# Performance work log

Measured on AMD Instinct MI355X. Metric: run time of the kernel, lower is better.

## Reference

```python
import jax, jax.numpy as jnp
import numpy as np

E, K, N, T = 8, 2048, 1024, 4096


def setup_inputs() -> dict:
    key = jax.random.key(0)
    kx, kw = jax.random.split(key)
    x = jax.random.normal(kx, (T, K), dtype=jnp.float32)
    weight = jax.random.normal(kw, (E, N, K), dtype=jnp.float32)
    # cumulative group end offsets per expert; equal split, offs[-1] == T
    offs = (jnp.arange(1, E + 1) * (T // E)).astype(jnp.int32)
    return {"x": x, "weight": weight, "offs": offs}


def reference(x, weight, offs):
    # torch: wt = weight.transpose(-2, -1); y = torch._grouped_mm(x, wt, offs)
    # Grouped GEMM over contiguous ragged token groups: tokens in
    # [starts[e], offs[e]) are multiplied by expert e's weight.
    wt = jnp.swapaxes(weight, -2, -1)  # [E, K, N]
    starts = jnp.concatenate([jnp.zeros((1,), offs.dtype), offs[:-1]])  # [E]
    tok = jnp.arange(x.shape[0], dtype=offs.dtype)[:, None]  # [T, 1]
    y = jnp.zeros((x.shape[0], wt.shape[-1]), dtype=x.dtype)
    for e in range(wt.shape[0]):  # fixed small expert count
        mask = (tok >= starts[e]) & (tok < offs[e])  # [T, 1]
        y = y + jnp.where(mask, x, jnp.zeros((), x.dtype)) @ wt[e]
    return y
```

## Files before the change

kernel.cpp:

```cpp
#include <hip/hip_runtime.h>
#include <hip/hip_bf16.h>

typedef __attribute__((ext_vector_type(4))) float f32x4;
typedef __attribute__((ext_vector_type(4))) unsigned int u32x4;
typedef __attribute__((ext_vector_type(8))) __bf16 bf16x8;

namespace {
constexpr int T_ = 4096;
constexpr int K_ = 2048;
constexpr int N_ = 1024;
constexpr int E_ = 8;
constexpr int BM = 128, BN = 128, BK = 32;
constexpr int LSTR = BK + 8;
constexpr size_t PART_ELEMS = (size_t)T_ * N_;
}

__device__ __forceinline__ unsigned int pk2(float a, float b) {
    union { __hip_bfloat162 h; unsigned int u; } c;
    c.h = __float22bfloat162_rn(make_float2(a, b));
    return c.u;
}

__device__ __forceinline__ u32x4 cvt8(f32x4 a, f32x4 b) {
    u32x4 r;
    r.x = pk2(a.x, a.y);
    r.y = pk2(a.z, a.w);
    r.z = pk2(b.x, b.y);
    r.w = pk2(b.z, b.w);
    return r;
}

template <int KSPLIT, int ATOMIC>
__global__ __launch_bounds__(256, 3) void gg_bf16_kernel(
        const float* __restrict__ x, const float* __restrict__ w,
        const int* __restrict__ offs, float* __restrict__ out) {
    constexpr int KCH = K_ / KSPLIT;
    constexpr int NKS = KCH / BK;
    __shared__ __align__(16) unsigned short As[2][BM * LSTR];
    __shared__ __align__(16) unsigned short Bs[2][BN * LSTR];

    const int tid = threadIdx.x;
    const int lane = tid & 63;
    const int wid = tid >> 6;
    const int wr = wid >> 1, wc = wid & 1;

    const int b = blockIdx.x;
    const int xcd = b & 7;
    const int inner = b >> 3;
    const int ks = inner >> 5;
    const int rem = inner & 31;
    const int by = xcd * 4 + (rem >> 3);
    const int bx = rem & 7;
    const int brow = by * BM;
    const int bcol = bx * BN;
    const int k0 = ks * KCH;

    float* outp = ATOMIC ? out : (out + (size_t)ks * PART_ELEMS);

    const int srow = tid >> 2;
    const int scol = (tid & 3) * 8;
    const float* aB0 = x + (size_t)(brow + srow) * K_ + k0 + scol;
    const float* aB1 = aB0 + (size_t)64 * K_;
    const int ldsO0 = srow * LSTR + scol;
    const int ldsO1 = (srow + 64) * LSTR + scol;

    const int frow = lane & 15;
    const int fk = (lane >> 4) * 8;
    const int aF = (wr * 64 + frow) * LSTR + fk;
    const int bF = (wc * 64 + frow) * LSTR + fk;

#define LOADT(t)                                                      \
    do {                                                              \
        const float* _a0 = aB0 + (t) * BK;                            \
        const float* _a1 = aB1 + (t) * BK;                            \
        const float* _b0 = bB0 + (t) * BK;                            \
        const float* _b1 = bB1 + (t) * BK;                            \
        ra0 = *(const f32x4*)_a0; ra1 = *(const f32x4*)(_a0 + 4);     \
        ra2 = *(const f32x4*)_a1; ra3 = *(const f32x4*)(_a1 + 4);     \
        rb0 = *(const f32x4*)_b0; rb1 = *(const f32x4*)(_b0 + 4);     \
        rb2 = *(const f32x4*)_b1; rb3 = *(const f32x4*)(_b1 + 4);     \
    } while (0)

#define STORET(buf)                                                   \
    do {                                                              \
        *(u32x4*)&As[buf][ldsO0] = cvt8(ra0, ra1);                    \
        *(u32x4*)&As[buf][ldsO1] = cvt8(ra2, ra3);                    \
        *(u32x4*)&Bs[buf][ldsO0] = cvt8(rb0, rb1);                    \
        *(u32x4*)&Bs[buf][ldsO1] = cvt8(rb2, rb3);                    \
    } while (0)

    for (int e = 0; e < E_; ++e) {
        const int s = (e == 0) ? 0 : offs[e - 1];
        const int en = offs[e];
        if (en <= brow || s >= brow + BM) continue;

        const float* bB0 = w + ((size_t)e * N_ + bcol + srow) * K_ + k0 + scol;
        const float* bB1 = bB0 + (size_t)64 * K_;

        f32x4 ra0, ra1, ra2, ra3, rb0, rb1, rb2, rb3;
        LOADT(0);
        STORET(0);
        LOADT(1);
        __syncthreads();

        f32x4 acc[4][4];
#pragma unroll
        for (int m = 0; m < 4; ++m)
#pragma unroll
            for (int n = 0; n < 4; ++n)
                acc[m][n] = f32x4{0.0f, 0.0f, 0.0f, 0.0f};

        for (int t = 0; t < NKS; ++t) {
            const int cur = t & 1;
            if (t + 1 < NKS) STORET(cur ^ 1);
            if (t + 2 < NKS) LOADT(t + 2);
            bf16x8 af[4], bg[4];
#pragma unroll
            for (int m = 0; m < 4; ++m)
                af[m] = *(const bf16x8*)&As[cur][aF + m * 16 * LSTR];
#pragma unroll
            for (int n = 0; n < 4; ++n)
                bg[n] = *(const bf16x8*)&Bs[cur][bF + n * 16 * LSTR];
#pragma unroll
            for (int m = 0; m < 4; ++m)
#pragma unroll
                for (int n = 0; n < 4; ++n)
                    acc[m][n] = __builtin_amdgcn_mfma_f32_16x16x32_bf16(
                        af[m], bg[n], acc[m][n], 0, 0, 0);
            __syncthreads();
        }

        const int cb = bcol + wc * 64 + frow;
#pragma unroll
        for (int m = 0; m < 4; ++m) {
            const int r0 = brow + wr * 64 + m * 16 + (lane >> 4) * 4;
#pragma unroll
            for (int r = 0; r < 4; ++r) {
                const int row = r0 + r;
                if (row < s || row >= en) continue;
                float* yp = outp + (size_t)row * N_ + cb;
#pragma unroll
                for (int n = 0; n < 4; ++n) {
                    if (ATOMIC) atomicAdd(&yp[n * 16], acc[m][n][r]);
                    else        yp[n * 16] = acc[m][n][r];
                }
            }
        }
        __syncthreads();
    }
#undef LOADT
#undef STORET
}

template <int P>
__global__ __launch_bounds__(256) void gg_reduce_kernel(
        const float* __restrict__ part, float* __restrict__ y) {
    const size_t i = (size_t)blockIdx.x * blockDim.x + threadIdx.x;
    f32x4 acc = ((const f32x4*)part)[i];
#pragma unroll
    for (int p = 1; p < P; ++p)
        acc += ((const f32x4*)(part + (size_t)p * PART_ELEMS))[i];
    ((f32x4*)y)[i] = acc;
}

extern "C" void kernel_launch(void* const* d_in, const int* in_sizes, int n_in,
                              void* d_out, int out_size, void* d_ws, size_t ws_size,
                              hipStream_t stream) {
    const float* x = (const float*)d_in[0];
    const float* w = (const float*)d_in[1];
    const int* offs = (const int*)d_in[2];
    float* y = (float*)d_out;
    float* part = (float*)d_ws;
    const int rgrid = (int)(PART_ELEMS / 4 / 256);

    if (ws_size >= 4 * PART_ELEMS * sizeof(float)) {
        gg_bf16_kernel<4, 0><<<dim3(256 * 4), dim3(256), 0, stream>>>(x, w, offs, part);
        gg_reduce_kernel<4><<<dim3(rgrid), dim3(256), 0, stream>>>(part, y);
    } else if (ws_size >= 2 * PART_ELEMS * sizeof(float)) {
        gg_bf16_kernel<2, 0><<<dim3(256 * 2), dim3(256), 0, stream>>>(x, w, offs, part);
        gg_reduce_kernel<2><<<dim3(rgrid), dim3(256), 0, stream>>>(part, y);
    } else {
        hipMemsetAsync(d_out, 0, PART_ELEMS * sizeof(float), stream);
        gg_bf16_kernel<2, 1><<<dim3(256 * 2), dim3(256), 0, stream>>>(x, w, offs, y);
    }
}
```

Before: 55.07 us.

## Pre-convert inputs to bf16 and stage tiles via direct global-to-LDS loads

```diff
diff --git a/kernel.cpp b/kernel.cpp
--- a/kernel.cpp
+++ b/kernel.cpp
@@ -4,6 +4,7 @@
 typedef __attribute__((ext_vector_type(4))) float f32x4;
 typedef __attribute__((ext_vector_type(4))) unsigned int u32x4;
 typedef __attribute__((ext_vector_type(8))) __bf16 bf16x8;
+using u16 = unsigned short;
 
 namespace {
 constexpr int T_ = 4096;
@@ -13,6 +14,8 @@
 constexpr int BM = 128, BN = 128, BK = 32;
 constexpr int LSTR = BK + 8;
 constexpr size_t PART_ELEMS = (size_t)T_ * N_;
+constexpr size_t XB_ELEMS = (size_t)T_ * K_;
+constexpr size_t WB_ELEMS = (size_t)E_ * N_ * K_;
 }
 
 __device__ __forceinline__ unsigned int pk2(float a, float b) {
@@ -30,14 +33,130 @@
     return r;
 }
 
+__device__ __forceinline__ void gld16(const u16* g, u16* l) {
+    __builtin_amdgcn_global_load_lds(
+        (const __attribute__((address_space(1))) void*)g,
+        (__attribute__((address_space(3))) void*)l, 16, 0, 0);
+}
+
+__global__ __launch_bounds__(256) void cvt_bf16_kernel(
+        const float* __restrict__ in, unsigned int* __restrict__ out, int n8) {
+    const int stride = gridDim.x * blockDim.x;
+    for (int i = blockIdx.x * blockDim.x + threadIdx.x; i < n8; i += stride) {
+        const f32x4 a = ((const f32x4*)in)[2 * i];
+        const f32x4 b = ((const f32x4*)in)[2 * i + 1];
+        ((u32x4*)out)[i] = cvt8(a, b);
+    }
+}
+
+template <int KSPLIT>
+__global__ __launch_bounds__(256) void gg_lds_kernel(
+        const u16* __restrict__ xb, const u16* __restrict__ wb,
+        const int* __restrict__ offs, float* __restrict__ out) {
+    constexpr int KCH = K_ / KSPLIT;
+    constexpr int NKS = KCH / BK;
+    __shared__ __align__(16) u16 As[2][BM * BK];
+    __shared__ __align__(16) u16 Bs[2][BN * BK];
+
+    const int tid = threadIdx.x;
+    const int lane = tid & 63;
+    const int wid = tid >> 6;
+    const int wr = wid >> 1, wc = wid & 1;
+
+    const int b = blockIdx.x;
+    const int xcd = b & 7;
+    const int inner = b >> 3;
+    const int ks = inner >> 5;
+    const int rem = inner & 31;
+    const int by = xcd * 4 + (rem >> 3);
+    const int bx = rem & 7;
+    const int brow = by * BM;
+    const int bcol = bx * BN;
+    const int k0 = ks * KCH;
+
+    float* outp = out + (size_t)ks * PART_ELEMS;
+
+    const int grow = tid >> 2;
+    const int gcol = (tid & 3) * 8;
+    const u16* aS = xb + (size_t)(brow + grow) * K_ + k0 + gcol;
+
+    const int frow = lane & 15;
+    const int fk = (lane >> 4) * 8;
+    const int aF = (wr * 64 + frow) * BK + fk;
+    const int bF = (wc * 64 + frow) * BK + fk;
+
+#define STAGE(t, buf)                                                  \
+    do {                                                               \
+        const u16* _a = aS + (t) * BK;                                 \
+        const u16* _b = bS + (t) * BK;                                 \
+        gld16(_a,                   &As[buf][tid * 8]);                \
+        gld16(_a + (size_t)64 * K_, &As[buf][2048 + tid * 8]);         \
+        gld16(_b,                   &Bs[buf][tid * 8]);                \
+        gld16(_b + (size_t)64 * K_, &Bs[buf][2048 + tid * 8]);         \
+    } while (0)
+
+    for (int e = 0; e < E_; ++e) {
+        const int s = (e == 0) ? 0 : offs[e - 1];
+        const int en = offs[e];
+        if (en <= brow || s >= brow + BM) continue;
+
+        const u16* bS = wb + ((size_t)e * N_ + bcol + grow) * K_ + k0 + gcol;
+
+        STAGE(0, 0);
+        __syncthreads();
+
+        f32x4 acc[4][4];
+#pragma unroll
+        for (int m = 0; m < 4; ++m)
+#pragma unroll
+            for (int n = 0; n < 4; ++n)
+                acc[m][n] = f32x4{0.0f, 0.0f, 0.0f, 0.0f};
+
+        for (int t = 0; t < NKS; ++t) {
+            const int cur = t & 1;
+            if (t + 1 < NKS) STAGE(t + 1, cur ^ 1);
+            bf16x8 af[4], bg[4];
+#pragma unroll
+            for (int m = 0; m < 4; ++m)
+                af[m] = *(const bf16x8*)&As[cur][aF + m * 16 * BK];
+#pragma unroll
+            for (int n = 0; n < 4; ++n)
+                bg[n] = *(const bf16x8*)&Bs[cur][bF + n * 16 * BK];
+#pragma unroll
+            for (int m = 0; m < 4; ++m)
+#pragma unroll
+                for (int n = 0; n < 4; ++n)
+                    acc[m][n] = __builtin_amdgcn_mfma_f32_16x16x32_bf16(
+                        af[m], bg[n], acc[m][n], 0, 0, 0);
+            __syncthreads();
+        }
+
+        const int cb = bcol + wc * 64 + frow;
+#pragma unroll
+        for (int m = 0; m < 4; ++m) {
+            const int r0 = brow + wr * 64 + m * 16 + (lane >> 4) * 4;
+#pragma unroll
+            for (int r = 0; r < 4; ++r) {
+                const int row = r0 + r;
+                if (row < s || row >= en) continue;
+                float* yp = outp + (size_t)row * N_ + cb;
+#pragma unroll
+                for (int n = 0; n < 4; ++n) yp[n * 16] = acc[m][n][r];
+            }
+        }
+        __syncthreads();
+    }
+#undef STAGE
+}
+
 template <int KSPLIT, int ATOMIC>
 __global__ __launch_bounds__(256, 3) void gg_bf16_kernel(
         const float* __restrict__ x, const float* __restrict__ w,
         const int* __restrict__ offs, float* __restrict__ out) {
     constexpr int KCH = K_ / KSPLIT;
     constexpr int NKS = KCH / BK;
-    __shared__ __align__(16) unsigned short As[2][BM * LSTR];
-    __shared__ __align__(16) unsigned short Bs[2][BN * LSTR];
+    __shared__ __align__(16) u16 As[2][BM * LSTR];
+    __shared__ __align__(16) u16 Bs[2][BN * LSTR];
 
     const int tid = threadIdx.x;
     const int lane = tid & 63;
@@ -173,14 +292,33 @@
     float* part = (float*)d_ws;
     const int rgrid = (int)(PART_ELEMS / 4 / 256);
 
-    if (ws_size >= 4 * PART_ELEMS * sizeof(float)) {
-        gg_bf16_kernel<4, 0><<<dim3(256 * 4), dim3(256), 0, stream>>>(x, w, offs, part);
+    const size_t bf16_bytes = (XB_ELEMS + WB_ELEMS) * sizeof(u16);
+    const size_t need4 = 4 * PART_ELEMS * sizeof(float) + bf16_bytes;
+    const size_t need2 = 2 * PART_ELEMS * sizeof(float) + bf16_bytes;
+
+    if (ws_size >= need4 || ws_size >= need2) {
+        const int ksplit = (ws_size >= need4) ? 4 : 2;
+        u16* xb = (u16*)(part + (size_t)ksplit * PART_ELEMS);
+        u16* wb = xb + XB_ELEMS;
+        cvt_bf16_kernel<<<dim3(2048), dim3(256), 0, stream>>>(
+            x, (unsigned int*)xb, (int)(XB_ELEMS / 8));
+        cvt_bf16_kernel<<<dim3(2048), dim3(256), 0, stream>>>(
+            w, (unsigned int*)wb, (int)(WB_ELEMS / 8));
+        if (ksplit == 4) {
+            gg_lds_kernel<4><<<dim3(1024), dim3(256), 0, stream>>>(xb, wb, offs, part);
+            gg_reduce_kernel<4><<<dim3(rgrid), dim3(256), 0, stream>>>(part, y);
+        } else {
+            gg_lds_kernel<2><<<dim3(512), dim3(256), 0, stream>>>(xb, wb, offs, part);
+            gg_reduce_kernel<2><<<dim3(rgrid), dim3(256), 0, stream>>>(part, y);
+        }
+    } else if (ws_size >= 4 * PART_ELEMS * sizeof(float)) {
+        gg_bf16_kernel<4, 0><<<dim3(1024), dim3(256), 0, stream>>>(x, w, offs, part);
         gg_reduce_kernel<4><<<dim3(rgrid), dim3(256), 0, stream>>>(part, y);
     } else if (ws_size >= 2 * PART_ELEMS * sizeof(float)) {
-        gg_bf16_kernel<2, 0><<<dim3(256 * 2), dim3(256), 0, stream>>>(x, w, offs, part);
+        gg_bf16_kernel<2, 0><<<dim3(512), dim3(256), 0, stream>>>(x, w, offs, part);
         gg_reduce_kernel<2><<<dim3(rgrid), dim3(256), 0, stream>>>(part, y);
     } else {
         hipMemsetAsync(d_out, 0, PART_ELEMS * sizeof(float), stream);
-        gg_bf16_kernel<2, 1><<<dim3(256 * 2), dim3(256), 0, stream>>>(x, w, offs, y);
+        gg_bf16_kernel<2, 1><<<dim3(512), dim3(256), 0, stream>>>(x, w, offs, y);
     }
 }
```

After: 77.67 us. 1.41x slower.
